# Kernel tuning notes

Hardware: AMD Instinct MI355X
Metric: run time of the kernel (lower is better)

The kernel has to match this reference:

```python
import jax, jax.numpy as jnp
import numpy as np

B, D, T, H, E = 4, 1024, 2048, 16, 64  # batch, dim, seq_len, n_heads, hidden_dim (H*E == D)


def setup_inputs() -> dict:
    key = jax.random.key(0)
    ks = jax.random.split(key, 6)
    x = jax.random.normal(ks[0], (B, D, T), dtype=jnp.float32)            # (b, e, t) layout
    Wp = jax.random.normal(ks[1], (H, E, D), dtype=jnp.float32) / np.sqrt(D)  # per-head proj weights
    bp = jax.random.normal(ks[2], (H, E), dtype=jnp.float32) * 0.01
    tw = jax.random.normal(ks[3], (H, T), dtype=jnp.float32) / np.sqrt(T)  # per-head Toeplitz kernel, tw[h,0]=diagonal
    Wo = jax.random.normal(ks[4], (D, D), dtype=jnp.float32) / np.sqrt(D)
    bo = jax.random.normal(ks[5], (D,), dtype=jnp.float32) * 0.01
    return {"x": x, "Wp": Wp, "bp": bp, "tw": tw, "Wo": Wo, "bo": bo}


def reference(x, Wp, bp, tw, Wo, bo):
    # x: (b, dim, t) -> (b, t, dim)
    xt = jnp.transpose(x, (0, 2, 1))
    # per-head projections: (b, h, e, t)
    proj = jnp.einsum('btd,hed->bhet', xt, Wp) + bp[None, :, :, None]
    # build per-head causal lower-triangular Toeplitz matrices: Tm[h, t, s] = tw[h, t-s] if s <= t else 0
    idx = jnp.arange(T)[:, None] - jnp.arange(T)[None, :]  # (t, s)
    Tm = jnp.where(idx >= 0, tw[:, jnp.clip(idx, 0)], 0.0)  # (h, t, s)
    # causal Toeplitz mixing along time per head
    mixed = jnp.einsum('hts,bhes->bhet', Tm, proj)          # (b, h, e, t)
    # concat heads on feature dim: (b, t, h*e) == (b, t, dim)
    cat = jnp.transpose(mixed, (0, 3, 1, 2)).reshape(B, T, H * E)
    out = cat @ Wo.T + bo                                   # out_proj: Linear(dim, dim)
    return jnp.transpose(out, (0, 2, 1))                    # back to (b, e, t)
```

## Files before the change

### kernel.cpp

```cpp
#include <hip/hip_runtime.h>
#include <cstdint>

#define NB 4
#define ND 1024
#define NT 2048
#define NH 16
#define NE 64

typedef __bf16 bf16x8 __attribute__((ext_vector_type(8)));
typedef float f32x4 __attribute__((ext_vector_type(4)));
typedef unsigned short us8 __attribute__((ext_vector_type(8)));

__device__ __forceinline__ unsigned short f2bf(float f) {
  unsigned u = __builtin_bit_cast(unsigned, f);
  return (unsigned short)((u + 0x7fffu + ((u >> 16) & 1u)) >> 16);
}

__device__ __forceinline__ void gload16(const void* g, void* l) {
  __builtin_amdgcn_global_load_lds(
      (const __attribute__((address_space(1))) void*)(uintptr_t)g,
      (__attribute__((address_space(3))) void*)(uintptr_t)l, 16, 0, 0);
}

__global__ void prep_kernel(const float* __restrict__ Wp, const float* __restrict__ Wo,
                            const float* __restrict__ tw,
                            unsigned short* __restrict__ WpB, unsigned short* __restrict__ WoB,
                            float* __restrict__ Gf) {
  int idx = blockIdx.x * 256 + threadIdx.x;
  int stride = gridDim.x * 256;
  for (int i = idx; i < ND * ND; i += stride) WpB[i] = f2bf(Wp[i]);
  for (int i = idx; i < ND * ND; i += stride) WoB[i] = f2bf(Wo[i]);
  for (int i = idx; i < NH * 2 * NT; i += stride) {
    int h = i >> 12, k = i & 4095;
    int d = k - (NT - 1);
    float v = 0.f;
    if (d >= 0 && d < NT) {
      unsigned short b = f2bf(tw[h * NT + d]);
      v = __builtin_bit_cast(float, (unsigned)b << 16);
    }
    Gf[i] = v;
  }
}

__global__ __launch_bounds__(256) void transpose_cast(const float* __restrict__ x,
                                                      unsigned short* __restrict__ xT) {
  __shared__ float tile[32][33];
  int tx = threadIdx.x & 31, ty = threadIdx.x >> 5;
  int t0 = blockIdx.x * 32, d0 = blockIdx.y * 32, b = blockIdx.z;
  const float* xb = x + (long)b * ND * NT;
#pragma unroll
  for (int k = 0; k < 4; ++k)
    tile[ty + 8 * k][tx] = xb[(long)(d0 + ty + 8 * k) * NT + t0 + tx];
  __syncthreads();
  unsigned short* xTb = xT + (long)b * NT * ND;
#pragma unroll
  for (int k = 0; k < 4; ++k)
    xTb[(long)(t0 + ty + 8 * k) * ND + d0 + tx] = f2bf(tile[tx][ty + 8 * k]);
}

template <bool OUT_BF16>
__global__ __launch_bounds__(256, 2) void gemm_bt(const unsigned short* __restrict__ A,
                                                  const unsigned short* __restrict__ Bt,
                                                  const float* __restrict__ bias,
                                                  void* __restrict__ Cb, long strideB,
                                                  long strideC) {
  const int M = 1024, N = 2048, K = 1024;
  (void)M;
  __shared__ __align__(16) unsigned short As[128 * 32];
  __shared__ __align__(16) unsigned short Bs[128 * 32];
  const int tid = threadIdx.x;
  const int lane = tid & 63;
  const int wid = tid >> 6;
  const int wm = (wid & 1) * 64, wn = (wid >> 1) * 64;
  const int m0 = blockIdx.y * 128, n0 = blockIdx.x * 128;
  const unsigned short* Bb = Bt + (long)blockIdx.z * strideB;
  const int mlo = lane & 15, q = lane >> 4;

  f32x4 acc[4][4] = {};
  for (int k0 = 0; k0 < K; k0 += 32) {
#pragma unroll
    for (int p = 0; p < 2; ++p) {
      int idx = p * 256 + tid;
      int row = idx >> 2, kc = (idx & 3) * 8;
      gload16(A + (long)(m0 + row) * K + k0 + kc, &As[idx * 8]);
      gload16(Bb + (long)(n0 + row) * K + k0 + kc, &Bs[idx * 8]);
    }
    __syncthreads();
    bf16x8 av[4], bv[4];
#pragma unroll
    for (int i = 0; i < 4; ++i) {
      av[i] = __builtin_bit_cast(bf16x8, *(const us8*)&As[(wm + i * 16 + mlo) * 32 + q * 8]);
      bv[i] = __builtin_bit_cast(bf16x8, *(const us8*)&Bs[(wn + i * 16 + mlo) * 32 + q * 8]);
    }
#pragma unroll
    for (int i = 0; i < 4; ++i)
#pragma unroll
      for (int j = 0; j < 4; ++j)
        acc[i][j] = __builtin_amdgcn_mfma_f32_16x16x32_bf16(av[i], bv[j], acc[i][j], 0, 0, 0);
    __syncthreads();
  }
#pragma unroll
  for (int i = 0; i < 4; ++i)
#pragma unroll
    for (int j = 0; j < 4; ++j)
#pragma unroll
      for (int r = 0; r < 4; ++r) {
        int gr = m0 + wm + i * 16 + q * 4 + r;
        int gc = n0 + wn + j * 16 + mlo;
        float v = acc[i][j][r] + bias[gr];
        if (OUT_BF16)
          ((unsigned short*)Cb)[(long)blockIdx.z * strideC + (long)gr * N + gc] = f2bf(v);
        else
          ((float*)Cb)[(long)blockIdx.z * strideC + (long)gr * N + gc] = v;
      }
}

__global__ __launch_bounds__(256, 2) void toeplitz(const unsigned short* __restrict__ proj,
                                                   const float* __restrict__ Gf,
                                                   unsigned short* __restrict__ mixedT) {
  __shared__ float Gs[2176];
  __shared__ __align__(16) unsigned short Bs[128 * 32];
  const int tid = threadIdx.x, lane = tid & 63, w = tid >> 6;
  const int t0 = blockIdx.x * 128, h = blockIdx.y, zb = blockIdx.z;
  const int mlo = lane & 15, q = lane >> 4;

  const float* Gh = Gf + h * 2 * NT;
  const int glen = t0 + 256;
  for (int i = tid; i < glen; i += 256) Gs[i] = Gh[NT - 128 + i];

  f32x4 acc[2][8] = {};
  const int kend = t0 + 128;
  for (int s0 = 0; s0 < kend; s0 += 32) {
#pragma unroll
    for (int p = 0; p < 2; ++p) {
      int idx = p * 256 + tid;
      int n = idx >> 2, kc = (idx & 3) * 8;
      int bb = n >> 6, e = n & 63;
      gload16(proj + ((long)(zb * 2 + bb) * ND + h * 64 + e) * NT + s0 + kc, &Bs[idx * 8]);
    }
    __syncthreads();
    bf16x8 av[2];
#pragma unroll
    for (int i = 0; i < 2; ++i) {
      int base = (t0 + w * 32 + i * 16 + mlo) - (s0 + q * 8) + 127;
      us8 au;
#pragma unroll
      for (int j = 0; j < 8; ++j)
        au[j] = (unsigned short)(__builtin_bit_cast(unsigned, Gs[base - j]) >> 16);
      av[i] = __builtin_bit_cast(bf16x8, au);
    }
    bf16x8 bv[8];
#pragma unroll
    for (int j = 0; j < 8; ++j)
      bv[j] = __builtin_bit_cast(bf16x8, *(const us8*)&Bs[(j * 16 + mlo) * 32 + q * 8]);
#pragma unroll
    for (int i = 0; i < 2; ++i)
#pragma unroll
      for (int j = 0; j < 8; ++j)
        acc[i][j] = __builtin_amdgcn_mfma_f32_16x16x32_bf16(av[i], bv[j], acc[i][j], 0, 0, 0);
    __syncthreads();
  }
#pragma unroll
  for (int i = 0; i < 2; ++i)
#pragma unroll
    for (int j = 0; j < 8; ++j)
#pragma unroll
      for (int r = 0; r < 4; ++r) {
        int t = t0 + w * 32 + i * 16 + q * 4 + r;
        int n = j * 16 + mlo;
        int bb = n >> 6, e = n & 63;
        mixedT[((long)(zb * 2 + bb) * NT + t) * ND + h * 64 + e] = f2bf(acc[i][j][r]);
      }
}

extern "C" void kernel_launch(void* const* d_in, const int* in_sizes, int n_in, void* d_out,
                              int out_size, void* d_ws, size_t ws_size, hipStream_t stream) {
  const float* x = (const float*)d_in[0];
  const float* Wp = (const float*)d_in[1];
  const float* bp = (const float*)d_in[2];
  const float* tw = (const float*)d_in[3];
  const float* Wo = (const float*)d_in[4];
  const float* bo = (const float*)d_in[5];
  float* out = (float*)d_out;

  char* ws = (char*)d_ws;
  unsigned short* xT = (unsigned short*)(ws);
  unsigned short* proj = (unsigned short*)(ws + (16ull << 20));
  unsigned short* WpB = (unsigned short*)(ws + (32ull << 20));
  unsigned short* WoB = (unsigned short*)(ws + (34ull << 20));
  float* Gf = (float*)(ws + (36ull << 20));

  prep_kernel<<<dim3(2048), 256, 0, stream>>>(Wp, Wo, tw, WpB, WoB, Gf);
  transpose_cast<<<dim3(NT / 32, ND / 32, NB), 256, 0, stream>>>(x, xT);
  gemm_bt<true><<<dim3(16, 8, NB), 256, 0, stream>>>(WpB, xT, bp, proj, (long)NT * ND,
                                                     (long)ND * NT);
  toeplitz<<<dim3(NT / 128, NH, NB / 2), 256, 0, stream>>>(proj, Gf, xT);
  gemm_bt<false><<<dim3(16, 8, NB), 256, 0, stream>>>(WoB, xT, bo, out, (long)NT * ND,
                                                      (long)ND * NT);
}
```

Measured before the change: 190.4 us.

## Precompute shifted bf16 Toeplitz rows and load A fragments directly from global

Prep now builds eight shifted, reversed bf16 copies of each head's Toeplitz kernel, so each lane's 8-element A fragment is one aligned 16-byte global load. This replaces the per-element LDS gather and bit-shifting of the float table. The toeplitz kernel also moves to a 2x2 wave tiling with a 4x4 MFMA accumulator, which gives each wave more A reuse. Blocks are launched in reverse time order so the longest causal blocks start first. The cost is extra prep work and uncached global reads of the Toeplitz table on every k step.

Result: slower. 232.3 us (+22.0%).

```diff
diff --git a/kernel.cpp b/kernel.cpp
--- a/kernel.cpp
+++ b/kernel.cpp
@@ -6,6 +6,7 @@
 #define NT 2048
 #define NH 16
 #define NE 64
+#define GLEN 2240
 
 typedef __bf16 bf16x8 __attribute__((ext_vector_type(8)));
 typedef float f32x4 __attribute__((ext_vector_type(4)));
@@ -25,20 +26,18 @@
 __global__ void prep_kernel(const float* __restrict__ Wp, const float* __restrict__ Wo,
                             const float* __restrict__ tw,
                             unsigned short* __restrict__ WpB, unsigned short* __restrict__ WoB,
-                            float* __restrict__ Gf) {
+                            unsigned short* __restrict__ Gr8) {
   int idx = blockIdx.x * 256 + threadIdx.x;
   int stride = gridDim.x * 256;
   for (int i = idx; i < ND * ND; i += stride) WpB[i] = f2bf(Wp[i]);
   for (int i = idx; i < ND * ND; i += stride) WoB[i] = f2bf(Wo[i]);
-  for (int i = idx; i < NH * 2 * NT; i += stride) {
-    int h = i >> 12, k = i & 4095;
-    int d = k - (NT - 1);
-    float v = 0.f;
-    if (d >= 0 && d < NT) {
-      unsigned short b = f2bf(tw[h * NT + d]);
-      v = __builtin_bit_cast(float, (unsigned)b << 16);
-    }
-    Gf[i] = v;
+  for (int i = idx; i < NH * 8 * GLEN; i += stride) {
+    int h = i / (8 * GLEN);
+    int rem = i - h * 8 * GLEN;
+    int r = rem / GLEN;
+    int c = rem - r * GLEN;
+    int src = c + r;
+    Gr8[i] = (src <= NT - 1) ? f2bf(tw[h * NT + (NT - 1) - src]) : (unsigned short)0;
   }
 }
 
@@ -64,8 +63,7 @@
                                                   const float* __restrict__ bias,
                                                   void* __restrict__ Cb, long strideB,
                                                   long strideC) {
-  const int M = 1024, N = 2048, K = 1024;
-  (void)M;
+  const int N = 2048, K = 1024;
   __shared__ __align__(16) unsigned short As[128 * 32];
   __shared__ __align__(16) unsigned short Bs[128 * 32];
   const int tid = threadIdx.x;
@@ -116,19 +114,20 @@
 }
 
 __global__ __launch_bounds__(256, 2) void toeplitz(const unsigned short* __restrict__ proj,
-                                                   const float* __restrict__ Gf,
+                                                   const unsigned short* __restrict__ Gr8,
                                                    unsigned short* __restrict__ mixedT) {
-  __shared__ float Gs[2176];
   __shared__ __align__(16) unsigned short Bs[128 * 32];
   const int tid = threadIdx.x, lane = tid & 63, w = tid >> 6;
-  const int t0 = blockIdx.x * 128, h = blockIdx.y, zb = blockIdx.z;
+  const int t0 = ((int)gridDim.x - 1 - (int)blockIdx.x) * 128;
+  const int h = blockIdx.y, zb = blockIdx.z;
   const int mlo = lane & 15, q = lane >> 4;
+  const int wt = (w & 1) * 64, wn = (w >> 1) * 64;
 
-  const float* Gh = Gf + h * 2 * NT;
-  const int glen = t0 + 256;
-  for (int i = tid; i < glen; i += 256) Gs[i] = Gh[NT - 128 + i];
+  const int r = (7 - mlo) & 7;
+  const unsigned short* gA =
+      Gr8 + (long)(h * 8 + r) * GLEN + ((NT - 1) - mlo - r) - t0 - wt + q * 8;
 
-  f32x4 acc[2][8] = {};
+  f32x4 acc[4][4] = {};
   const int kend = t0 + 128;
   for (int s0 = 0; s0 < kend; s0 += 32) {
 #pragma unroll
@@ -139,37 +138,30 @@
       gload16(proj + ((long)(zb * 2 + bb) * ND + h * 64 + e) * NT + s0 + kc, &Bs[idx * 8]);
     }
     __syncthreads();
-    bf16x8 av[2];
+    bf16x8 av[4], bv[4];
 #pragma unroll
-    for (int i = 0; i < 2; ++i) {
-      int base = (t0 + w * 32 + i * 16 + mlo) - (s0 + q * 8) + 127;
-      us8 au;
+    for (int i = 0; i < 4; ++i)
+      av[i] = __builtin_bit_cast(bf16x8, *(const us8*)(gA + s0 - i * 16));
 #pragma unroll
-      for (int j = 0; j < 8; ++j)
-        au[j] = (unsigned short)(__builtin_bit_cast(unsigned, Gs[base - j]) >> 16);
-      av[i] = __builtin_bit_cast(bf16x8, au);
-    }
-    bf16x8 bv[8];
+    for (int j = 0; j < 4; ++j)
+      bv[j] = __builtin_bit_cast(bf16x8, *(const us8*)&Bs[(wn + j * 16 + mlo) * 32 + q * 8]);
 #pragma unroll
-    for (int j = 0; j < 8; ++j)
-      bv[j] = __builtin_bit_cast(bf16x8, *(const us8*)&Bs[(j * 16 + mlo) * 32 + q * 8]);
+    for (int i = 0; i < 4; ++i)
 #pragma unroll
-    for (int i = 0; i < 2; ++i)
-#pragma unroll
-      for (int j = 0; j < 8; ++j)
+      for (int j = 0; j < 4; ++j)
         acc[i][j] = __builtin_amdgcn_mfma_f32_16x16x32_bf16(av[i], bv[j], acc[i][j], 0, 0, 0);
     __syncthreads();
   }
 #pragma unroll
-  for (int i = 0; i < 2; ++i)
+  for (int i = 0; i < 4; ++i)
 #pragma unroll
-    for (int j = 0; j < 8; ++j)
+    for (int j = 0; j < 4; ++j)
 #pragma unroll
-      for (int r = 0; r < 4; ++r) {
-        int t = t0 + w * 32 + i * 16 + q * 4 + r;
-        int n = j * 16 + mlo;
+      for (int rr = 0; rr < 4; ++rr) {
+        int t = t0 + wt + i * 16 + q * 4 + rr;
+        int n = wn + j * 16 + mlo;
         int bb = n >> 6, e = n & 63;
-        mixedT[((long)(zb * 2 + bb) * NT + t) * ND + h * 64 + e] = f2bf(acc[i][j][r]);
+        mixedT[((long)(zb * 2 + bb) * NT + t) * ND + h * 64 + e] = f2bf(acc[i][j][rr]);
       }
 }
 
@@ -188,13 +180,13 @@
   unsigned short* proj = (unsigned short*)(ws + (16ull << 20));
   unsigned short* WpB = (unsigned short*)(ws + (32ull << 20));
   unsigned short* WoB = (unsigned short*)(ws + (34ull << 20));
-  float* Gf = (float*)(ws + (36ull << 20));
+  unsigned short* Gr8 = (unsigned short*)(ws + (36ull << 20));
 
-  prep_kernel<<<dim3(2048), 256, 0, stream>>>(Wp, Wo, tw, WpB, WoB, Gf);
+  prep_kernel<<<dim3(2048), 256, 0, stream>>>(Wp, Wo, tw, WpB, WoB, Gr8);
   transpose_cast<<<dim3(NT / 32, ND / 32, NB), 256, 0, stream>>>(x, xT);
   gemm_bt<true><<<dim3(16, 8, NB), 256, 0, stream>>>(WpB, xT, bp, proj, (long)NT * ND,
                                                      (long)ND * NT);
-  toeplitz<<<dim3(NT / 128, NH, NB / 2), 256, 0, stream>>>(proj, Gf, xT);
+  toeplitz<<<dim3(NT / 128, NH, NB / 2), 256, 0, stream>>>(proj, Gr8, xT);
   gemm_bt<false><<<dim3(16, 8, NB), 256, 0, stream>>>(WoB, xT, bo, out, (long)NT * ND,
                                                       (long)ND * NT);
 }
```
